# Optimization experiments

Hardware: AMD Instinct MI355X
Metric: run time of the kernel (lower is better)

## Reference

```python
import jax, jax.numpy as jnp
import numpy as np

N_NODES = 100000


def gcn_conv(x, edge_index, edge_weight, W, b):
    """PyG GCNConv: add self-loops (weight 1), symmetric deg^-1/2 norm,
    linear transform, scatter-add aggregation over destination nodes, + bias."""
    n = x.shape[0]
    src = jnp.concatenate([edge_index[0], jnp.arange(n, dtype=edge_index.dtype)])
    dst = jnp.concatenate([edge_index[1], jnp.arange(n, dtype=edge_index.dtype)])
    ew = jnp.concatenate([edge_weight, jnp.ones((n,), dtype=x.dtype)])
    # weighted degree over destinations (symmetric graph assumed as in GCN norm)
    deg = jax.ops.segment_sum(ew, dst, num_segments=n)
    dinv = jnp.where(deg > 0, jax.lax.rsqrt(deg), 0.0).astype(x.dtype)
    norm = dinv[src] * ew * dinv[dst]                    # [E+N]
    h = x @ W                                            # [N, out]
    msg = h[src] * norm[:, None]                         # gather + scale
    agg = jax.ops.segment_sum(msg, dst, num_segments=n)  # scatter-add
    return agg + b


def setup_inputs() -> dict:
    key = jax.random.key(0)
    k = jax.random.split(key, 8)
    d_in, d_hid, d_out = 128, 64, 2
    n_edges = 3200000
    x = jax.random.normal(k[0], (N_NODES, d_in), dtype=jnp.float32)
    edge_index = jax.random.randint(k[1], (2, n_edges), 0, N_NODES, dtype=jnp.int64)
    edge_weight = jax.random.uniform(k[2], (n_edges,), dtype=jnp.float32)
    # Glorot-ish init for linear weights, zeros for bias (PyG default)
    W1 = jax.random.normal(k[3], (d_in, d_hid), dtype=jnp.float32) / np.sqrt(d_in)
    b1 = jnp.zeros((d_hid,), dtype=jnp.float32)
    W2 = jax.random.normal(k[4], (d_hid, d_out), dtype=jnp.float32) / np.sqrt(d_hid)
    b2 = jnp.zeros((d_out,), dtype=jnp.float32)
    return {"x": x, "edge_index": edge_index, "edge_weight": edge_weight,
            "W1": W1, "b1": b1, "W2": W2, "b2": b2}


def reference(x, edge_index, edge_weight, W1, b1, W2, b2):
    h = gcn_conv(x, edge_index, edge_weight, W1, b1)
    h = jax.nn.relu(h)
    out = gcn_conv(h, edge_index, edge_weight, W2, b2)
    return out
```

## Files before the change

kernel.cpp:

```cpp
#include <hip/hip_runtime.h>
#include <hip/hip_bf16.h>
#include <hip/hip_fp16.h>


#define DIN  128
#define DHID 64
#define BSH  7
#define BCAP 5000

typedef _Float16 half8 __attribute__((ext_vector_type(8)));
typedef float    f32x4 __attribute__((ext_vector_type(4)));

__global__ __launch_bounds__(256) void k_hist(const int* __restrict__ ei,
                                              int* __restrict__ histT,
                                              int E, int chunk, int B, int C) {
    extern __shared__ int h[];
    for (int t = threadIdx.x; t < B; t += 256) h[t] = 0;
    __syncthreads();
    int c = blockIdx.x;
    int e0 = c * chunk, e1 = min(E, e0 + chunk);
    for (int e = e0 + threadIdx.x; e < e1; e += 256)
        atomicAdd(&h[ei[E + e] >> BSH], 1);
    __syncthreads();
    for (int t = threadIdx.x; t < B; t += 256) histT[(size_t)t * C + c] = h[t];
}

__global__ __launch_bounds__(256) void k_scan1(int* __restrict__ histT,
                                               int* __restrict__ tot, int C) {
    __shared__ int sm[256];
    int b = blockIdx.x, t = threadIdx.x;
    size_t base = (size_t)b * C;
    int v = histT[base + t];
    sm[t] = v;
    __syncthreads();
    for (int off = 1; off < 256; off <<= 1) {
        int add = (t >= off) ? sm[t - off] : 0;
        __syncthreads();
        sm[t] += add;
        __syncthreads();
    }
    histT[base + t] = sm[t] - v;
    if (t == 255) tot[b] = sm[t];
}

__global__ __launch_bounds__(1024) void k_scan2(const int* __restrict__ tot,
                                                int* __restrict__ bb, int B) {
    __shared__ int sm[1024];
    int t = threadIdx.x;
    int v = (t < B) ? tot[t] : 0;
    sm[t] = v;
    __syncthreads();
    for (int off = 1; off < 1024; off <<= 1) {
        int add = (t >= off) ? sm[t - off] : 0;
        __syncthreads();
        sm[t] += add;
        __syncthreads();
    }
    if (t < B) {
        bb[t] = sm[t] - v;
        if (t == B - 1) bb[B] = sm[t];
    }
}

__global__ __launch_bounds__(256) void k_scatter(const int* __restrict__ ei,
                                                 const float* __restrict__ ew,
                                                 const int* __restrict__ histT,
                                                 const int* __restrict__ bb,
                                                 int2* __restrict__ ebuf,
                                                 int E, int chunk, int B, int C) {
    extern __shared__ int cur[];
    int c = blockIdx.x;
    for (int t = threadIdx.x; t < B; t += 256)
        cur[t] = histT[(size_t)t * C + c] + bb[t];
    __syncthreads();
    int e0 = c * chunk, e1 = min(E, e0 + chunk);
    for (int e = e0 + threadIdx.x; e < e1; e += 256) {
        int s = ei[e];
        int d = ei[E + e];
        float w = ew[e];
        int b = d >> BSH;
        int pos = atomicAdd(&cur[b], 1);
        ebuf[pos] = make_int2(s | ((d & 127) << 24), __float_as_int(w));
    }
}

__global__ __launch_bounds__(256) void k_build(const int2* __restrict__ ebuf,
                                               const int* __restrict__ bb,
                                               int* __restrict__ rp,
                                               float* __restrict__ dinv,
                                               int2* __restrict__ csw,
                                               int N, int E) {
    __shared__ int2  stage[BCAP];
    __shared__ int   cnt[128];
    __shared__ float dsum[128];
    __shared__ int   lrp[128];
    __shared__ int   cur[128];
    __shared__ int   sm[128];
    int b = blockIdx.x, t = threadIdx.x;
    if (t < 128) { cnt[t] = 0; dsum[t] = 0.0f; cur[t] = 0; }
    __syncthreads();
    int p0 = bb[b], p1 = bb[b + 1];
    int m = p1 - p0;
    bool fits = (m <= BCAP);
    for (int p = p0 + t; p < p1; p += 256) {
        int2 v = ebuf[p];
        if (fits) stage[p - p0] = v;
        int ln = (((unsigned)v.x) >> 24) & 127;
        atomicAdd(&cnt[ln], 1);
        atomicAdd(&dsum[ln], __int_as_float(v.y));
    }
    __syncthreads();
    if (t < 128) {
        int cv = cnt[t];
        sm[t] = cv;
        __syncthreads();
        for (int off = 1; off < 128; off <<= 1) {
            int add = (t >= off) ? sm[t - off] : 0;
            __syncthreads();
            sm[t] += add;
            __syncthreads();
        }
        lrp[t] = sm[t] - cv + p0;
        int d = (b << BSH) + t;
        if (d < N) {
            rp[d]   = lrp[t];
            dinv[d] = rsqrtf(1.0f + dsum[t]);
        }
        if (b == 0 && t == 0) rp[N] = E;
    } else {
        __syncthreads();
        for (int off = 1; off < 128; off <<= 1) { __syncthreads(); __syncthreads(); }
    }
    __syncthreads();
    for (int q = t; q < m; q += 256) {
        int2 v = fits ? stage[q] : ebuf[p0 + q];
        int ln = (((unsigned)v.x) >> 24) & 127;
        int r = atomicAdd(&cur[ln], 1);
        csw[lrp[ln] + r] = make_int2(v.x & 0xFFFFFF, v.y);
    }
}

__global__ __launch_bounds__(256) void k_gemm1(const float* __restrict__ x,
                                               const float* __restrict__ W1,
                                               __half* __restrict__ h1, int N) {
    __shared__ _Float16 As[64][136];
    __shared__ _Float16 Bs[64][136];
    int t = threadIdx.x;
    int wave = t >> 6, lane = t & 63;
    int r0 = blockIdx.x * 64;

    for (int idx = t; idx < DIN * DHID; idx += 256) {
        int k = idx >> 6, c = idx & 63;
        Bs[c][k] = (_Float16)W1[idx];
    }
    const float4* xv = (const float4*)x;
    for (int idx = t; idx < 64 * 32; idx += 256) {
        int r = idx >> 5, c4 = idx & 31;
        int rr = r0 + r;
        float4 v = (rr < N) ? xv[(size_t)rr * 32 + c4]
                            : make_float4(0.f, 0.f, 0.f, 0.f);
        As[r][c4 * 4 + 0] = (_Float16)v.x;
        As[r][c4 * 4 + 1] = (_Float16)v.y;
        As[r][c4 * 4 + 2] = (_Float16)v.z;
        As[r][c4 * 4 + 3] = (_Float16)v.w;
    }
    __syncthreads();

    int row = lane & 15;
    int kg  = lane >> 4;
    f32x4 acc0 = {0.f,0.f,0.f,0.f}, acc1 = {0.f,0.f,0.f,0.f};
    f32x4 acc2 = {0.f,0.f,0.f,0.f}, acc3 = {0.f,0.f,0.f,0.f};
#pragma unroll
    for (int kc = 0; kc < 4; ++kc) {
        half8 a = *(const half8*)&As[wave * 16 + row][kc * 32 + kg * 8];
        half8 b0 = *(const half8*)&Bs[ 0 + row][kc * 32 + kg * 8];
        half8 b1 = *(const half8*)&Bs[16 + row][kc * 32 + kg * 8];
        half8 b2 = *(const half8*)&Bs[32 + row][kc * 32 + kg * 8];
        half8 b3 = *(const half8*)&Bs[48 + row][kc * 32 + kg * 8];
        acc0 = __builtin_amdgcn_mfma_f32_16x16x32_f16(a, b0, acc0, 0, 0, 0);
        acc1 = __builtin_amdgcn_mfma_f32_16x16x32_f16(a, b1, acc1, 0, 0, 0);
        acc2 = __builtin_amdgcn_mfma_f32_16x16x32_f16(a, b2, acc2, 0, 0, 0);
        acc3 = __builtin_amdgcn_mfma_f32_16x16x32_f16(a, b3, acc3, 0, 0, 0);
    }
#pragma unroll
    for (int reg = 0; reg < 4; ++reg) {
        int rr = r0 + wave * 16 + kg * 4 + reg;
        if (rr < N) {
            int col = lane & 15;
            size_t base = (size_t)rr * DHID;
            h1[base + col +  0] = __float2half(acc0[reg]);
            h1[base + col + 16] = __float2half(acc1[reg]);
            h1[base + col + 32] = __float2half(acc2[reg]);
            h1[base + col + 48] = __float2half(acc3[reg]);
        }
    }
}

__global__ __launch_bounds__(256) void k_agg1(const __half* __restrict__ h1h,
                                              const int* __restrict__ rp,
                                              const int2* __restrict__ csw,
                                              const float* __restrict__ dinv,
                                              const float* __restrict__ b1,
                                              const float* __restrict__ W2,
                                              float* __restrict__ h2, int N) {
    int lane = threadIdx.x & 63;
    int i = (blockIdx.x * 256 + threadIdx.x) >> 6;
    if (i >= N) return;
    float bias = b1[lane];
    float w2a = W2[lane * 2];
    float w2b = W2[lane * 2 + 1];
    int s0 = __builtin_amdgcn_readfirstlane(rp[i]);
    int e0 = __builtin_amdgcn_readfirstlane(rp[i + 1]);
    float acc = 0.0f;
    int p = s0;
    for (; p + 8 <= e0; p += 8) {
        int2 eA = csw[p],     eB = csw[p + 1], eC = csw[p + 2], eD = csw[p + 3];
        int2 eE = csw[p + 4], eF = csw[p + 5], eG = csw[p + 6], eH = csw[p + 7];
        int sA = __builtin_amdgcn_readfirstlane(eA.x);
        int sB = __builtin_amdgcn_readfirstlane(eB.x);
        int sC = __builtin_amdgcn_readfirstlane(eC.x);
        int sD = __builtin_amdgcn_readfirstlane(eD.x);
        int sE = __builtin_amdgcn_readfirstlane(eE.x);
        int sF = __builtin_amdgcn_readfirstlane(eF.x);
        int sG = __builtin_amdgcn_readfirstlane(eG.x);
        int sH = __builtin_amdgcn_readfirstlane(eH.x);
        float wA = __uint_as_float(__builtin_amdgcn_readfirstlane(eA.y)) * dinv[sA];
        float wB = __uint_as_float(__builtin_amdgcn_readfirstlane(eB.y)) * dinv[sB];
        float wC = __uint_as_float(__builtin_amdgcn_readfirstlane(eC.y)) * dinv[sC];
        float wD = __uint_as_float(__builtin_amdgcn_readfirstlane(eD.y)) * dinv[sD];
        float wE = __uint_as_float(__builtin_amdgcn_readfirstlane(eE.y)) * dinv[sE];
        float wF = __uint_as_float(__builtin_amdgcn_readfirstlane(eF.y)) * dinv[sF];
        float wG = __uint_as_float(__builtin_amdgcn_readfirstlane(eG.y)) * dinv[sG];
        float wH = __uint_as_float(__builtin_amdgcn_readfirstlane(eH.y)) * dinv[sH];
        float hA = __half2float(h1h[(size_t)sA * DHID + lane]);
        float hB = __half2float(h1h[(size_t)sB * DHID + lane]);
        float hC = __half2float(h1h[(size_t)sC * DHID + lane]);
        float hD = __half2float(h1h[(size_t)sD * DHID + lane]);
        float hE = __half2float(h1h[(size_t)sE * DHID + lane]);
        float hF = __half2float(h1h[(size_t)sF * DHID + lane]);
        float hG = __half2float(h1h[(size_t)sG * DHID + lane]);
        float hH = __half2float(h1h[(size_t)sH * DHID + lane]);
        acc = fmaf(wA, hA, acc);
        acc = fmaf(wB, hB, acc);
        acc = fmaf(wC, hC, acc);
        acc = fmaf(wD, hD, acc);
        acc = fmaf(wE, hE, acc);
        acc = fmaf(wF, hF, acc);
        acc = fmaf(wG, hG, acc);
        acc = fmaf(wH, hH, acc);
    }
    for (; p + 4 <= e0; p += 4) {
        int2 eA = csw[p], eB = csw[p + 1], eC = csw[p + 2], eD = csw[p + 3];
        int sA = __builtin_amdgcn_readfirstlane(eA.x);
        int sB = __builtin_amdgcn_readfirstlane(eB.x);
        int sC = __builtin_amdgcn_readfirstlane(eC.x);
        int sD = __builtin_amdgcn_readfirstlane(eD.x);
        float wA = __uint_as_float(__builtin_amdgcn_readfirstlane(eA.y)) * dinv[sA];
        float wB = __uint_as_float(__builtin_amdgcn_readfirstlane(eB.y)) * dinv[sB];
        float wC = __uint_as_float(__builtin_amdgcn_readfirstlane(eC.y)) * dinv[sC];
        float wD = __uint_as_float(__builtin_amdgcn_readfirstlane(eD.y)) * dinv[sD];
        float hA = __half2float(h1h[(size_t)sA * DHID + lane]);
        float hB = __half2float(h1h[(size_t)sB * DHID + lane]);
        float hC = __half2float(h1h[(size_t)sC * DHID + lane]);
        float hD = __half2float(h1h[(size_t)sD * DHID + lane]);
        acc = fmaf(wA, hA, acc);
        acc = fmaf(wB, hB, acc);
        acc = fmaf(wC, hC, acc);
        acc = fmaf(wD, hD, acc);
    }
    for (; p < e0; ++p) {
        int2 eA = csw[p];
        int sA = __builtin_amdgcn_readfirstlane(eA.x);
        float wA = __uint_as_float(__builtin_amdgcn_readfirstlane(eA.y)) * dinv[sA];
        acc = fmaf(wA, __half2float(h1h[(size_t)sA * DHID + lane]), acc);
    }
    float di = dinv[i];
    acc = (acc + di * __half2float(h1h[(size_t)i * DHID + lane])) * di;
    acc = fmaxf(acc + bias, 0.0f);
    float o0 = acc * w2a, o1 = acc * w2b;
    for (int off = 32; off > 0; off >>= 1) {
        o0 += __shfl_xor(o0, off);
        o1 += __shfl_xor(o1, off);
    }
    if (lane == 0) {
        h2[i * 2]     = o0;
        h2[i * 2 + 1] = o1;
    }
}

__global__ __launch_bounds__(256) void k_prop2(const float* __restrict__ h2,
                                               const int* __restrict__ rp,
                                               const int2* __restrict__ csw,
                                               const float* __restrict__ dinv,
                                               const float* __restrict__ b2,
                                               float* __restrict__ out, int N) {
    const float2* h2v = (const float2*)h2;
    int lane = threadIdx.x & 63;
    int i = (blockIdx.x * 256 + threadIdx.x) >> 6;
    if (i >= N) return;
    float b20 = b2[0], b21 = b2[1];
    int s0 = rp[i], e0 = rp[i + 1];
    float a0 = 0.0f, a1 = 0.0f;
    for (int p = s0 + lane; p < e0; p += 64) {
        int2 ed = csw[p];
        float w = __int_as_float(ed.y) * dinv[ed.x];
        float2 hv = h2v[ed.x];
        a0 = fmaf(w, hv.x, a0);
        a1 = fmaf(w, hv.y, a1);
    }
    for (int off = 32; off > 0; off >>= 1) {
        a0 += __shfl_xor(a0, off);
        a1 += __shfl_xor(a1, off);
    }
    if (lane == 0) {
        float di = dinv[i];
        out[i * 2]     = di * (a0 + di * h2[i * 2])     + b2[0];
        out[i * 2 + 1] = di * (a1 + di * h2[i * 2 + 1]) + b2[1];
    }
}

extern "C" void kernel_launch(void* const* d_in, const int* in_sizes, int n_in,
                              void* d_out, int out_size, void* d_ws, size_t ws_size,
                              hipStream_t stream) {
    const float* x  = (const float*)d_in[0];
    const int*   ei = (const int*)d_in[1];
    const float* ew = (const float*)d_in[2];
    const float* W1 = (const float*)d_in[3];
    const float* b1 = (const float*)d_in[4];
    const float* W2 = (const float*)d_in[5];
    const float* b2 = (const float*)d_in[6];
    float* out = (float*)d_out;

    const int N = in_sizes[0] / DIN;
    const int E = in_sizes[2];

    const int C = 256;
    const int B = (N + 127) >> BSH;
    const int chunk = (E + C - 1) / C;

    char* w0 = (char*)d_ws;
    float* dinv  = (float*)w0;
    int*   rp    = (int*)(dinv + N);
    int*   histT = rp + (N + 4);
    int*   tot   = histT + (size_t)B * C;
    int*   bb    = tot + B;
    size_t off_csw = ((size_t)((char*)(bb + B + 1) - w0) + 15) & ~(size_t)15;
    int2*  csw  = (int2*)(w0 + off_csw);
    int2*  ebuf = csw + E;
    __half* h1  = (__half*)ebuf;
    float* h2   = (float*)(h1 + (size_t)N * DHID);

    size_t ldsB = (size_t)B * sizeof(int);

    k_hist<<<C, 256, ldsB, stream>>>(ei, histT, E, chunk, B, C);
    k_scan1<<<B, 256, 0, stream>>>(histT, tot, C);
    k_scan2<<<1, 1024, 0, stream>>>(tot, bb, B);
    k_scatter<<<C, 256, ldsB, stream>>>(ei, ew, histT, bb, ebuf, E, chunk, B, C);
    k_build<<<B, 256, 0, stream>>>(ebuf, bb, rp, dinv, csw, N, E);

    const int GB = (N + 63) / 64;
    k_gemm1<<<GB, 256, 0, stream>>>(x, W1, h1, N);

    const int GW = ((size_t)N * 64 + 255) / 256;
    k_agg1<<<GW, 256, 0, stream>>>(h1, rp, csw, dinv, b1, W2, h2, N);
    k_prop2<<<GW, 256, 0, stream>>>(h2, rp, csw, dinv, b2, out, N);
}
```

Before: 379.5 us.

## Locally sort edges by bucket in LDS before scattering to ebuf

The scatter kernel now does a block-local counting sort of its edge chunk in shared memory, so writes to the bucketed edge buffer come out contiguous per bucket instead of being randomly interleaved through global atomics. The histogram and scatter kernels move to 1024-thread blocks, and the build kernel moves to 512 threads with a simplified uniform scan. The aim is to coalesce the scattered global writes. The cost is an extra pass over the destination indices and a large shared-memory footprint, and the code assumes each chunk fits in SCHUNK and B is at most BMAX.

```diff
diff --git a/kernel.cpp b/kernel.cpp
--- a/kernel.cpp
+++ b/kernel.cpp
@@ -7,22 +7,24 @@
 #define DHID 64
 #define BSH  7
 #define BCAP 5000
+#define SCHUNK 12544
+#define BMAX 800
 
 typedef _Float16 half8 __attribute__((ext_vector_type(8)));
 typedef float    f32x4 __attribute__((ext_vector_type(4)));
 
-__global__ __launch_bounds__(256) void k_hist(const int* __restrict__ ei,
-                                              int* __restrict__ histT,
-                                              int E, int chunk, int B, int C) {
+__global__ __launch_bounds__(1024) void k_hist(const int* __restrict__ ei,
+                                               int* __restrict__ histT,
+                                               int E, int chunk, int B, int C) {
     extern __shared__ int h[];
-    for (int t = threadIdx.x; t < B; t += 256) h[t] = 0;
+    for (int t = threadIdx.x; t < B; t += 1024) h[t] = 0;
     __syncthreads();
     int c = blockIdx.x;
     int e0 = c * chunk, e1 = min(E, e0 + chunk);
-    for (int e = e0 + threadIdx.x; e < e1; e += 256)
+    for (int e = e0 + threadIdx.x; e < e1; e += 1024)
         atomicAdd(&h[ei[E + e] >> BSH], 1);
     __syncthreads();
-    for (int t = threadIdx.x; t < B; t += 256) histT[(size_t)t * C + c] = h[t];
+    for (int t = threadIdx.x; t < B; t += 1024) histT[(size_t)t * C + c] = h[t];
 }
 
 __global__ __launch_bounds__(256) void k_scan1(int* __restrict__ histT,
@@ -62,29 +64,57 @@
     }
 }
 
-__global__ __launch_bounds__(256) void k_scatter(const int* __restrict__ ei,
-                                                 const float* __restrict__ ew,
-                                                 const int* __restrict__ histT,
-                                                 const int* __restrict__ bb,
-                                                 int2* __restrict__ ebuf,
-                                                 int E, int chunk, int B, int C) {
-    extern __shared__ int cur[];
-    int c = blockIdx.x;
-    for (int t = threadIdx.x; t < B; t += 256)
-        cur[t] = histT[(size_t)t * C + c] + bb[t];
-    __syncthreads();
-    int e0 = c * chunk, e1 = min(E, e0 + chunk);
-    for (int e = e0 + threadIdx.x; e < e1; e += 256) {
+__global__ __launch_bounds__(1024) void k_scatter(const int* __restrict__ ei,
+                                                  const float* __restrict__ ew,
+                                                  const int* __restrict__ histT,
+                                                  const int* __restrict__ bb,
+                                                  int2* __restrict__ ebuf,
+                                                  int E, int chunk, int B, int C) {
+    __shared__ int eidx[SCHUNK];
+    __shared__ int lbase[BMAX];
+    __shared__ int lcur[BMAX];
+    __shared__ int gbase[BMAX];
+    int c = blockIdx.x, t = threadIdx.x;
+    int e0 = c * chunk, e1 = min(E, e0 + chunk), m = e1 - e0;
+
+    for (int b = t; b < B; b += 1024) lcur[b] = 0;
+    __syncthreads();
+    for (int q = t; q < m; q += 1024)
+        atomicAdd(&lcur[ei[E + e0 + q] >> BSH], 1);
+    __syncthreads();
+    int v = (t < B) ? lcur[t] : 0;
+    eidx[t] = v;
+    __syncthreads();
+    for (int off = 1; off < 1024; off <<= 1) {
+        int add = (t >= off) ? eidx[t - off] : 0;
+        __syncthreads();
+        eidx[t] += add;
+        __syncthreads();
+    }
+    if (t < B) {
+        lbase[t] = eidx[t] - v;
+        gbase[t] = histT[(size_t)t * C + c] + bb[t];
+        lcur[t] = 0;
+    }
+    __syncthreads();
+    for (int q = t; q < m; q += 1024) {
+        int b = ei[E + e0 + q] >> BSH;
+        int pos = lbase[b] + atomicAdd(&lcur[b], 1);
+        eidx[pos] = q;
+    }
+    __syncthreads();
+    for (int q = t; q < m; q += 1024) {
+        int e = e0 + eidx[q];
         int s = ei[e];
         int d = ei[E + e];
         float w = ew[e];
         int b = d >> BSH;
-        int pos = atomicAdd(&cur[b], 1);
-        ebuf[pos] = make_int2(s | ((d & 127) << 24), __float_as_int(w));
-    }
-}
-
-__global__ __launch_bounds__(256) void k_build(const int2* __restrict__ ebuf,
+        int gpos = gbase[b] + (q - lbase[b]);
+        ebuf[gpos] = make_int2(s | ((d & 127) << 24), __float_as_int(w));
+    }
+}
+
+__global__ __launch_bounds__(512) void k_build(const int2* __restrict__ ebuf,
                                                const int* __restrict__ bb,
                                                int* __restrict__ rp,
                                                float* __restrict__ dinv,
@@ -95,14 +125,14 @@
     __shared__ float dsum[128];
     __shared__ int   lrp[128];
     __shared__ int   cur[128];
-    __shared__ int   sm[128];
+    __shared__ int   sm[512];
     int b = blockIdx.x, t = threadIdx.x;
     if (t < 128) { cnt[t] = 0; dsum[t] = 0.0f; cur[t] = 0; }
     __syncthreads();
     int p0 = bb[b], p1 = bb[b + 1];
     int m = p1 - p0;
     bool fits = (m <= BCAP);
-    for (int p = p0 + t; p < p1; p += 256) {
+    for (int p = p0 + t; p < p1; p += 512) {
         int2 v = ebuf[p];
         if (fits) stage[p - p0] = v;
         int ln = (((unsigned)v.x) >> 24) & 127;
@@ -110,29 +140,26 @@
         atomicAdd(&dsum[ln], __int_as_float(v.y));
     }
     __syncthreads();
+    int cv = (t < 128) ? cnt[t] : 0;
+    sm[t] = cv;
+    __syncthreads();
+    for (int off = 1; off < 128; off <<= 1) {
+        int add = (t >= off) ? sm[t - off] : 0;
+        __syncthreads();
+        sm[t] += add;
+        __syncthreads();
+    }
     if (t < 128) {
-        int cv = cnt[t];
-        sm[t] = cv;
-        __syncthreads();
-        for (int off = 1; off < 128; off <<= 1) {
-            int add = (t >= off) ? sm[t - off] : 0;
-            __syncthreads();
-            sm[t] += add;
-            __syncthreads();
-        }
         lrp[t] = sm[t] - cv + p0;
         int d = (b << BSH) + t;
         if (d < N) {
             rp[d]   = lrp[t];
             dinv[d] = rsqrtf(1.0f + dsum[t]);
         }
-        if (b == 0 && t == 0) rp[N] = E;
-    } else {
-        __syncthreads();
-        for (int off = 1; off < 128; off <<= 1) { __syncthreads(); __syncthreads(); }
-    }
-    __syncthreads();
-    for (int q = t; q < m; q += 256) {
+    }
+    if (b == 0 && t == 0) rp[N] = E;
+    __syncthreads();
+    for (int q = t; q < m; q += 512) {
         int2 v = fits ? stage[q] : ebuf[p0 + q];
         int ln = (((unsigned)v.x) >> 24) & 127;
         int r = atomicAdd(&cur[ln], 1);
@@ -298,7 +325,6 @@
     int lane = threadIdx.x & 63;
     int i = (blockIdx.x * 256 + threadIdx.x) >> 6;
     if (i >= N) return;
-    float b20 = b2[0], b21 = b2[1];
     int s0 = rp[i], e0 = rp[i + 1];
     float a0 = 0.0f, a1 = 0.0f;
     for (int p = s0 + lane; p < e0; p += 64) {
@@ -352,11 +378,11 @@
 
     size_t ldsB = (size_t)B * sizeof(int);
 
-    k_hist<<<C, 256, ldsB, stream>>>(ei, histT, E, chunk, B, C);
+    k_hist<<<C, 1024, ldsB, stream>>>(ei, histT, E, chunk, B, C);
     k_scan1<<<B, 256, 0, stream>>>(histT, tot, C);
     k_scan2<<<1, 1024, 0, stream>>>(tot, bb, B);
-    k_scatter<<<C, 256, ldsB, stream>>>(ei, ew, histT, bb, ebuf, E, chunk, B, C);
-    k_build<<<B, 256, 0, stream>>>(ebuf, bb, rp, dinv, csw, N, E);
+    k_scatter<<<C, 1024, 0, stream>>>(ei, ew, histT, bb, ebuf, E, chunk, B, C);
+    k_build<<<B, 512, 0, stream>>>(ebuf, bb, rp, dinv, csw, N, E);
 
     const int GB = (N + 63) / 64;
     k_gemm1<<<GB, 256, 0, stream>>>(x, W1, h1, N);
```

New measurement: 377.1 us. No clear change (-0.6%).
